# Performance work log

Hardware: AMD Instinct MI355X
Metric: run time of the kernel (lower is better)

The kernel has to match this reference:

```python
import jax, jax.numpy as jnp
import numpy as np

B, N, D, DC, R = 32, 36, 2048, 4, 512  # batch, regions, feat dim, coord dim, fusion rank


def setup_inputs() -> dict:
    key = jax.random.key(0)
    ks = jax.random.split(key, 8)
    s = lambda fan_in: 1.0 / np.sqrt(fan_in)
    return {
        "mm": jax.random.normal(ks[0], (B, N, D), dtype=jnp.float32),
        "coords": jax.random.uniform(ks[1], (B, N, DC), dtype=jnp.float32),
        "U_feat": jax.random.normal(ks[2], (D, R), dtype=jnp.float32) * s(D),
        "V_feat": jax.random.normal(ks[3], (D, R), dtype=jnp.float32) * s(D),
        "P_feat": jax.random.normal(ks[4], (R, D), dtype=jnp.float32) * s(R),
        "U_coord": jax.random.normal(ks[5], (DC, R), dtype=jnp.float32) * s(DC),
        "V_coord": jax.random.normal(ks[6], (DC, R), dtype=jnp.float32) * s(DC),
        "P_coord": jax.random.normal(ks[7], (R, D), dtype=jnp.float32) * s(R),
    }


def reference(mm, coords, U_feat, V_feat, P_feat, U_coord, V_coord, P_coord):
    # Pairwise module: build all (i, j) region pairs, fuse, max-aggregate over j.
    # Original torch code detach_()'s the gathered pair tensors -> stop_gradient here.
    mm_sg = jax.lax.stop_gradient(mm)
    coords_sg = jax.lax.stop_gradient(coords)

    # Coord fusion (MLB-style low-rank multiplicative fusion)
    uc = jnp.einsum("bnc,cr->bnr", coords_sg, U_coord)   # [B,N,R]
    vc = jnp.einsum("bnc,cr->bnr", coords_sg, V_coord)   # [B,N,R]
    zc = jax.nn.relu(uc[:, :, None, :] * vc[:, None, :, :])  # [B,N,N,R]
    Rij = jnp.einsum("bijr,rd->bijd", zc, P_coord)       # [B,N,N,D]

    # Feature fusion
    uf = jnp.einsum("bnd,dr->bnr", mm_sg, U_feat)
    vf = jnp.einsum("bnd,dr->bnr", mm_sg, V_feat)
    zf = jax.nn.relu(uf[:, :, None, :] * vf[:, None, :, :])  # [B,N,N,R]
    Rij = Rij + jnp.einsum("bijr,rd->bijd", zf, P_feat)  # [B,N,N,D]

    # agg['type'] == 'max': reduce over the second region axis (j)
    mm_new = jnp.max(Rij, axis=2)                        # [B,N,D]

    # residual
    return mm_new + mm
```

## Files before the change

kernel.cpp:

```cpp
#include <hip/hip_runtime.h>

#define BI    1152
#define NREG  36
#define DD    2048
#define RR    512
#define KK    1024
#define ZROWS (BI*NREG)
#define MBLK  288
#define NBLK  128
#define ABUF  (MBLK*32)
#define BBUF  (NBLK*32)
#define BUFE  (ABUF+BBUF)

typedef __bf16 bf16;
typedef __bf16 bf16x8 __attribute__((ext_vector_type(8)));
typedef __bf16 bf16x4 __attribute__((ext_vector_type(4)));
typedef float  f32x4  __attribute__((ext_vector_type(4)));

__device__ __forceinline__ void gl_lds16(const void* g, void* l) {
  __builtin_amdgcn_global_load_lds(
      (const __attribute__((address_space(1))) unsigned int*)g,
      (__attribute__((address_space(3))) unsigned int*)l, 16, 0, 0);
}

__global__ void k_prep(const float* __restrict__ mm, const float* __restrict__ coords,
                       const float* __restrict__ U_feat, const float* __restrict__ V_feat,
                       const float* __restrict__ P_feat, const float* __restrict__ U_coord,
                       const float* __restrict__ V_coord, const float* __restrict__ P_coord,
                       bf16* __restrict__ mmb, bf16* __restrict__ UT, bf16* __restrict__ VT,
                       bf16* __restrict__ PTt, float* __restrict__ uc, float* __restrict__ vc) {
  __shared__ float tile[32][33];
  int bid = blockIdx.x, tid = threadIdx.x;
  if (bid < 2304) {
    int i = bid * 256 + tid;
    float4 v = ((const float4*)mm)[i];
    bf16x4 o = {(bf16)v.x, (bf16)v.y, (bf16)v.z, (bf16)v.w};
    ((bf16x4*)mmb)[i] = o;
  } else if (bid < 4352) {
    int rel = bid - 2304;
    int zz = rel >> 10, rr = rel & 1023;
    int c0 = (rr & 15) * 32, r0 = (rr >> 4) * 32;
    const float* in = zz ? V_feat : U_feat;
    bf16* outp = zz ? VT : UT;
    int tx = tid & 31, ty = tid >> 5;
#pragma unroll
    for (int k = 0; k < 4; k++)
      tile[ty + 8 * k][tx] = in[(long)(r0 + ty + 8 * k) * 512 + c0 + tx];
    __syncthreads();
#pragma unroll
    for (int k = 0; k < 4; k++)
      outp[(long)(c0 + ty + 8 * k) * 2048 + r0 + tx] = (bf16)tile[tx][ty + 8 * k];
  } else if (bid < 6400) {
    int rel = bid - 4352;
    int zz = rel >> 10, rr = rel & 1023;
    int c0 = (rr & 63) * 32, r0 = (rr >> 6) * 32;
    const float* in = zz ? P_feat : P_coord;
    int koff = zz * 512;
    int tx = tid & 31, ty = tid >> 5;
#pragma unroll
    for (int k = 0; k < 4; k++)
      tile[ty + 8 * k][tx] = in[(long)(r0 + ty + 8 * k) * 2048 + c0 + tx];
    __syncthreads();
    int kc = (koff + r0) >> 5;
#pragma unroll
    for (int k = 0; k < 4; k++) {
      int d = c0 + ty + 8 * k;
      PTt[((long)kc * 2048 + d) * 32 + tx] = (bf16)tile[tx][ty + 8 * k];
    }
  } else {
    int g = bid - 6400;
    float c0 = coords[g * 4 + 0], c1 = coords[g * 4 + 1];
    float c2 = coords[g * 4 + 2], c3 = coords[g * 4 + 3];
#pragma unroll
    for (int i = 0; i < 2; i++) {
      int r = tid + i * 256;
      uc[g * RR + r] = c0 * U_coord[r] + c1 * U_coord[RR + r] + c2 * U_coord[2 * RR + r] + c3 * U_coord[3 * RR + r];
      vc[g * RR + r] = c0 * V_coord[r] + c1 * V_coord[RR + r] + c2 * V_coord[2 * RR + r] + c3 * V_coord[3 * RR + r];
    }
  }
}

__launch_bounds__(256)
__global__ void k_gemm_uv(const bf16* __restrict__ mmb, const bf16* __restrict__ UT,
                          const bf16* __restrict__ VT, float* __restrict__ uf,
                          float* __restrict__ vf) {
  __shared__ bf16 lds2[2][6144];
  const bf16* Bmat = blockIdx.z ? VT : UT;
  float* outp = blockIdx.z ? vf : uf;
  int m0 = blockIdx.x * 64, n0 = blockIdx.y * 128;
  int tid = threadIdx.x, wave = tid >> 6, lane = tid & 63;
  int l15 = lane & 15, qv = lane >> 4;
  int qp_c = qv ^ ((l15 >> 1) & 3);
  int qs = (lane & 3) ^ ((lane >> 3) & 3);

  const bf16* gA = mmb + (long)(m0 + wave * 16 + (lane >> 2)) * 2048 + qs * 8;
  const bf16* gB = Bmat + (long)(n0 + wave * 32 + (lane >> 2)) * 2048 + qs * 8;
  int lA = wave * 512;
  int lB = 2048 + wave * 1024;

  auto stage = [&](int buf, int k0) {
    bf16* db = &lds2[buf][0];
    gl_lds16(gA + k0, db + lA);
    gl_lds16(gB + k0, db + lB);
    gl_lds16(gB + 16 * 2048 + k0, db + lB + 512);
  };

  f32x4 acc[4][2] = {};
  stage(0, 0);
  for (int k0 = 0; k0 < 2048; k0 += 32) {
    int cur = (k0 >> 5) & 1;
    __syncthreads();
    if (k0 + 32 < 2048) stage(cur ^ 1, k0 + 32);
    bf16x8 a[4], b[2];
#pragma unroll
    for (int mt = 0; mt < 4; mt++)
      a[mt] = *(const bf16x8*)(&lds2[cur][0] + (mt * 16 + l15) * 32 + qp_c * 8);
#pragma unroll
    for (int nt = 0; nt < 2; nt++)
      b[nt] = *(const bf16x8*)(&lds2[cur][2048] + (wave * 32 + nt * 16 + l15) * 32 + qp_c * 8);
#pragma unroll
    for (int mt = 0; mt < 4; mt++)
#pragma unroll
      for (int nt = 0; nt < 2; nt++)
        acc[mt][nt] = __builtin_amdgcn_mfma_f32_16x16x32_bf16(a[mt], b[nt], acc[mt][nt], 0, 0, 0);
  }
#pragma unroll
  for (int mt = 0; mt < 4; mt++)
#pragma unroll
    for (int nt = 0; nt < 2; nt++)
#pragma unroll
      for (int r = 0; r < 4; r++) {
        int row = m0 + mt * 16 + qv * 4 + r;
        int col = n0 + wave * 32 + nt * 16 + l15;
        outp[(long)row * RR + col] = acc[mt][nt][r];
      }
}

__global__ void k_build_z(const float* __restrict__ uc, const float* __restrict__ vc,
                          const float* __restrict__ uf, const float* __restrict__ vf,
                          bf16* __restrict__ z) {
  __shared__ float uL[36 * 128];
  __shared__ float vL[36 * 128];
  int kq = blockIdx.x, b = blockIdx.y, tid = threadIdx.x;
  const float* usrc = (kq < 4) ? uc : uf;
  const float* vsrc = (kq < 4) ? vc : vf;
  int kb = (kq & 3) * 128;
  for (int i = tid; i < 1152; i += 256) {
    int row = i >> 5, kk = (i & 31) * 4;
    long src = (long)(b * 36 + row) * RR + kb + kk;
    *(float4*)&uL[row * 128 + kk] = *(const float4*)(usrc + src);
    *(float4*)&vL[row * 128 + kk] = *(const float4*)(vsrc + src);
  }
  __syncthreads();
  for (int c = tid; c < 41472; c += 256) {
    int kcl = c / 10368;
    int rem = c - kcl * 10368;
    int row = rem >> 3;
    int x4 = rem & 7;
    int gl = row / 36;
    int j = row - gl * 36;
    int kl = kcl * 32 + x4 * 4;
    float4 u4 = *(const float4*)&uL[gl * 128 + kl];
    float4 v4 = *(const float4*)&vL[j * 128 + kl];
    float x0 = fmaxf(u4.x * v4.x, 0.f), x1 = fmaxf(u4.y * v4.y, 0.f);
    float x2 = fmaxf(u4.z * v4.z, 0.f), x3 = fmaxf(u4.w * v4.w, 0.f);
    bf16x4 o = {(bf16)x0, (bf16)x1, (bf16)x2, (bf16)x3};
    int bi = b * 36 + gl;
    long rowp = (long)(bi >> 3) * 288 + j * 8 + (bi & 7);
    *(bf16x4*)(z + ((long)(kq * 4 + kcl) * ZROWS + rowp) * 32 + x4 * 4) = o;
  }
}

__launch_bounds__(384, 3)
__global__ void k_main(const bf16* __restrict__ z, const bf16* __restrict__ PTt,
                       const float* __restrict__ mm, float* __restrict__ out) {
  __shared__ bf16 lds[2 * BUFE];
  int bid = blockIdx.x;
  int x = bid & 7, dt = (bid >> 3) & 15, chunk = bid >> 7;
  int go = chunk * 8 + x;
  int d0 = dt * NBLK;
  int tid = threadIdx.x, wave = tid / 64, lane = tid & 63;
  int l15 = lane & 15, qv = lane >> 4;
  int qp_c = qv ^ ((l15 >> 1) & 3);
  int ws = wave >> 1;
  int nh = wave & 1;

  int qs = (lane & 3) ^ ((lane >> 3) & 3);
  int lroff = (lane >> 2) * 32 + qs * 8;

  const bf16* gA = z + (long)go * (MBLK * 32) + wave * 1536 + lroff;
  const bf16* gB = PTt + (long)d0 * 32 + wave * 1024 + lroff;
  int lA = wave * 1536;
  int lB = ABUF + wave * 1024;

  int sbuf = 0;
  auto stage = [&]() {
    bf16* db = lds + sbuf * BUFE;
    gl_lds16(gA, db + lA);
    gl_lds16(gA + 512, db + lA + 512);
    gl_lds16(gA + 1024, db + lA + 1024);
    gA += (long)ZROWS * 32;
    if (wave < 4) {
      gl_lds16(gB, db + lB);
      gl_lds16(gB + 512, db + lB + 512);
      gB += 2048L * 32;
    }
    sbuf ^= 1;
  };

  f32x4 acc[6][4] = {};
  stage();
  for (int kc = 0; kc < 32; kc++) {
    __syncthreads();
    if (kc < 31) stage();
    const bf16* cur = lds + (kc & 1) * BUFE;
    bf16x8 a[6], b[4];
#pragma unroll
    for (int mt = 0; mt < 6; mt++)
      a[mt] = *(const bf16x8*)(cur + (ws * 96 + mt * 16 + l15) * 32 + qp_c * 8);
#pragma unroll
    for (int nt = 0; nt < 4; nt++)
      b[nt] = *(const bf16x8*)(cur + ABUF + (nh * 64 + nt * 16 + l15) * 32 + qp_c * 8);
#pragma unroll
    for (int mt = 0; mt < 6; mt++)
#pragma unroll
      for (int nt = 0; nt < 4; nt++)
        acc[mt][nt] = __builtin_amdgcn_mfma_f32_16x16x32_bf16(a[mt], b[nt], acc[mt][nt], 0, 0, 0);
  }

  float* pf = (float*)lds;
#pragma unroll
  for (int nt = 0; nt < 4; nt++) {
    int col = nh * 64 + nt * 16 + l15;
    float mx[4];
#pragma unroll
    for (int r = 0; r < 4; r++) {
      mx[r] = acc[0][nt][r];
#pragma unroll
      for (int mt = 1; mt < 6; mt++) mx[r] = fmaxf(mx[r], acc[mt][nt][r]);
      mx[r] = fmaxf(mx[r], __shfl_xor(mx[r], 32, 64));
    }
    if (qv == 0) {
#pragma unroll
      for (int r = 0; r < 4; r++) pf[(ws * 8 + r) * 128 + col] = mx[r];
    } else if (qv == 1) {
#pragma unroll
      for (int r = 0; r < 4; r++) pf[(ws * 8 + 4 + r) * 128 + col] = mx[r];
    }
  }
  __syncthreads();
  for (int o = tid; o < 1024; o += 384) {
    int gl = o >> 7, col = o & 127;
    float v = fmaxf(fmaxf(pf[gl * 128 + col], pf[(8 + gl) * 128 + col]),
                    pf[(16 + gl) * 128 + col]);
    long oa = (long)(go * 8 + gl) * DD + d0 + col;
    out[oa] = v + mm[oa];
  }
}

extern "C" void kernel_launch(void* const* d_in, const int* in_sizes, int n_in,
                              void* d_out, int out_size, void* d_ws, size_t ws_size,
                              hipStream_t stream) {
  const float* mm     = (const float*)d_in[0];
  const float* coords = (const float*)d_in[1];
  const float* U_feat = (const float*)d_in[2];
  const float* V_feat = (const float*)d_in[3];
  const float* P_feat = (const float*)d_in[4];
  const float* U_coord= (const float*)d_in[5];
  const float* V_coord= (const float*)d_in[6];
  const float* P_coord= (const float*)d_in[7];
  float* out = (float*)d_out;

  char* ws = (char*)d_ws;
  bf16* z   = (bf16*)(ws + 0);
  bf16* PTt = (bf16*)(ws + 84934656);
  bf16* mmb = (bf16*)(ws + 89128960);
  bf16* UT  = (bf16*)(ws + 93847552);
  bf16* VT  = (bf16*)(ws + 95944704);
  float* uf = (float*)(ws + 98041856);
  float* vf = (float*)(ws + 100401152);
  float* uc = (float*)(ws + 102760448);
  float* vc = (float*)(ws + 105119744);

  k_prep<<<dim3(7552), dim3(256), 0, stream>>>(mm, coords, U_feat, V_feat, P_feat,
                                               U_coord, V_coord, P_coord,
                                               mmb, UT, VT, PTt, uc, vc);
  k_gemm_uv<<<dim3(18, 4, 2), dim3(256), 0, stream>>>(mmb, UT, VT, uf, vf);
  k_build_z<<<dim3(8, 32), dim3(256), 0, stream>>>(uc, vc, uf, vf, z);
  k_main<<<dim3(2304), dim3(384), 0, stream>>>(z, PTt, mm, out);
}
```

Baseline: 302.1 us.

## Reshape main GEMM tile to 144x256 with 4 waves and in-register max reduction

Changes the main fused GEMM+max kernel from a 288x128 tile with 6 waves to a 144x256 tile with 4 waves. Each wave now covers all 144 rows (4 output groups x 36 pairs) for its 64 columns, so the max over j finishes with register shuffles and no LDS/barrier epilogue. The z layout in the build kernel is changed to 4-group interleaving to match. Each wave holds 9x4 accumulators, which raises register pressure and lowers waves per block. Staging traffic also shifts toward the B operand.

```diff
diff --git a/kernel.cpp b/kernel.cpp
--- a/kernel.cpp
+++ b/kernel.cpp
@@ -6,8 +6,8 @@
 #define RR    512
 #define KK    1024
 #define ZROWS (BI*NREG)
-#define MBLK  288
-#define NBLK  128
+#define MBLK  144
+#define NBLK  256
 #define ABUF  (MBLK*32)
 #define BBUF  (NBLK*32)
 #define BUFE  (ABUF+BBUF)
@@ -166,95 +166,84 @@
     float x2 = fmaxf(u4.z * v4.z, 0.f), x3 = fmaxf(u4.w * v4.w, 0.f);
     bf16x4 o = {(bf16)x0, (bf16)x1, (bf16)x2, (bf16)x3};
     int bi = b * 36 + gl;
-    long rowp = (long)(bi >> 3) * 288 + j * 8 + (bi & 7);
+    long rowp = (long)(bi >> 2) * 144 + j * 4 + (bi & 3);
     *(bf16x4*)(z + ((long)(kq * 4 + kcl) * ZROWS + rowp) * 32 + x4 * 4) = o;
   }
 }
 
-__launch_bounds__(384, 3)
+__launch_bounds__(256, 2)
 __global__ void k_main(const bf16* __restrict__ z, const bf16* __restrict__ PTt,
                        const float* __restrict__ mm, float* __restrict__ out) {
   __shared__ bf16 lds[2 * BUFE];
   int bid = blockIdx.x;
-  int x = bid & 7, dt = (bid >> 3) & 15, chunk = bid >> 7;
-  int go = chunk * 8 + x;
+  int x = bid & 7, t = bid >> 3;
+  int dt = t & 7, go = (t >> 3) * 8 + x;
   int d0 = dt * NBLK;
-  int tid = threadIdx.x, wave = tid / 64, lane = tid & 63;
+  int tid = threadIdx.x, wave = tid >> 6, lane = tid & 63;
   int l15 = lane & 15, qv = lane >> 4;
   int qp_c = qv ^ ((l15 >> 1) & 3);
-  int ws = wave >> 1;
-  int nh = wave & 1;
 
   int qs = (lane & 3) ^ ((lane >> 3) & 3);
   int lroff = (lane >> 2) * 32 + qs * 8;
 
-  const bf16* gA = z + (long)go * (MBLK * 32) + wave * 1536 + lroff;
-  const bf16* gB = PTt + (long)d0 * 32 + wave * 1024 + lroff;
-  int lA = wave * 1536;
-  int lB = ABUF + wave * 1024;
+  const bf16* gA = z + (long)go * ABUF + wave * 1024 + lroff;
+  const bf16* gB = PTt + (long)d0 * 32 + wave * 2048 + lroff;
+  int lA = wave * 1024;
+  int lB = ABUF + wave * 2048;
 
   int sbuf = 0;
   auto stage = [&]() {
     bf16* db = lds + sbuf * BUFE;
     gl_lds16(gA, db + lA);
     gl_lds16(gA + 512, db + lA + 512);
-    gl_lds16(gA + 1024, db + lA + 1024);
+    if (wave == 0) gl_lds16(gA + 4096, db + 4096);
+    gl_lds16(gB, db + lB);
+    gl_lds16(gB + 512, db + lB + 512);
+    gl_lds16(gB + 1024, db + lB + 1024);
+    gl_lds16(gB + 1536, db + lB + 1536);
     gA += (long)ZROWS * 32;
-    if (wave < 4) {
-      gl_lds16(gB, db + lB);
-      gl_lds16(gB + 512, db + lB + 512);
-      gB += 2048L * 32;
-    }
+    gB += 2048L * 32;
     sbuf ^= 1;
   };
 
-  f32x4 acc[6][4] = {};
+  f32x4 acc[9][4] = {};
   stage();
   for (int kc = 0; kc < 32; kc++) {
     __syncthreads();
     if (kc < 31) stage();
     const bf16* cur = lds + (kc & 1) * BUFE;
-    bf16x8 a[6], b[4];
-#pragma unroll
-    for (int mt = 0; mt < 6; mt++)
-      a[mt] = *(const bf16x8*)(cur + (ws * 96 + mt * 16 + l15) * 32 + qp_c * 8);
+    bf16x8 b[4];
 #pragma unroll
     for (int nt = 0; nt < 4; nt++)
-      b[nt] = *(const bf16x8*)(cur + ABUF + (nh * 64 + nt * 16 + l15) * 32 + qp_c * 8);
-#pragma unroll
-    for (int mt = 0; mt < 6; mt++)
+      b[nt] = *(const bf16x8*)(cur + ABUF + (wave * 64 + nt * 16 + l15) * 32 + qp_c * 8);
+#pragma unroll
+    for (int mt = 0; mt < 9; mt++) {
+      bf16x8 av = *(const bf16x8*)(cur + (mt * 16 + l15) * 32 + qp_c * 8);
 #pragma unroll
       for (int nt = 0; nt < 4; nt++)
-        acc[mt][nt] = __builtin_amdgcn_mfma_f32_16x16x32_bf16(a[mt], b[nt], acc[mt][nt], 0, 0, 0);
-  }
-
-  float* pf = (float*)lds;
+        acc[mt][nt] = __builtin_amdgcn_mfma_f32_16x16x32_bf16(av, b[nt], acc[mt][nt], 0, 0, 0);
+    }
+  }
+
 #pragma unroll
   for (int nt = 0; nt < 4; nt++) {
-    int col = nh * 64 + nt * 16 + l15;
     float mx[4];
 #pragma unroll
     for (int r = 0; r < 4; r++) {
       mx[r] = acc[0][nt][r];
 #pragma unroll
-      for (int mt = 1; mt < 6; mt++) mx[r] = fmaxf(mx[r], acc[mt][nt][r]);
+      for (int mt = 1; mt < 9; mt++) mx[r] = fmaxf(mx[r], acc[mt][nt][r]);
+      mx[r] = fmaxf(mx[r], __shfl_xor(mx[r], 16, 64));
       mx[r] = fmaxf(mx[r], __shfl_xor(mx[r], 32, 64));
     }
-    if (qv == 0) {
-#pragma unroll
-      for (int r = 0; r < 4; r++) pf[(ws * 8 + r) * 128 + col] = mx[r];
-    } else if (qv == 1) {
-#pragma unroll
-      for (int r = 0; r < 4; r++) pf[(ws * 8 + 4 + r) * 128 + col] = mx[r];
-    }
-  }
-  __syncthreads();
-  for (int o = tid; o < 1024; o += 384) {
-    int gl = o >> 7, col = o & 127;
-    float v = fmaxf(fmaxf(pf[gl * 128 + col], pf[(8 + gl) * 128 + col]),
-                    pf[(16 + gl) * 128 + col]);
-    long oa = (long)(go * 8 + gl) * DD + d0 + col;
-    out[oa] = v + mm[oa];
+    if (lane < 16) {
+      int col = d0 + wave * 64 + nt * 16 + lane;
+#pragma unroll
+      for (int r = 0; r < 4; r++) {
+        long oa = (long)(go * 4 + r) * DD + col;
+        out[oa] = mx[r] + mm[oa];
+      }
+    }
   }
 }
 
@@ -287,5 +276,5 @@
                                                mmb, UT, VT, PTt, uc, vc);
   k_gemm_uv<<<dim3(18, 4, 2), dim3(256), 0, stream>>>(mmb, UT, VT, uf, vf);
   k_build_z<<<dim3(8, 32), dim3(256), 0, stream>>>(uc, vc, uf, vf, z);
-  k_main<<<dim3(2304), dim3(384), 0, stream>>>(z, PTt, mm, out);
-}
+  k_main<<<dim3(2304), dim3(256), 0, stream>>>(z, PTt, mm, out);
+}
```

After: 259.7 us. 1.16x faster.
